# Kernel optimization log

Measured on AMD Instinct MI355X. Metric: run time of the kernel, lower is better.

## Reference

```python
import jax, jax.numpy as jnp
import numpy as np

N = 100000      # nodes
E = 1600000     # edges
F = 128         # num_node_features
H = 128         # hidden_channels
C = 10          # num_classes
R = 2           # num relations
G = 512         # num graphs in the batch


def setup_inputs() -> dict:
    key = jax.random.key(0)
    ks = jax.random.split(key, 16)
    s = 0.05
    x = jax.random.normal(ks[0], (N, F), dtype=jnp.float32)
    edge_index = jax.random.randint(ks[1], (2, E), 0, N, dtype=jnp.int64)
    edge_attr = jax.random.randint(ks[2], (E,), 0, R, dtype=jnp.int64)
    batch = jnp.sort(jax.random.randint(ks[3], (N,), 0, G, dtype=jnp.int64))
    W1 = jax.random.normal(ks[4], (R, F, H), dtype=jnp.float32) * s
    root1 = jax.random.normal(ks[5], (F, H), dtype=jnp.float32) * s
    b1 = jnp.zeros((H,), dtype=jnp.float32)
    W2 = jax.random.normal(ks[6], (R, H, H), dtype=jnp.float32) * s
    root2 = jax.random.normal(ks[7], (H, H), dtype=jnp.float32) * s
    b2 = jnp.zeros((H,), dtype=jnp.float32)
    W3 = jax.random.normal(ks[8], (R, H, H), dtype=jnp.float32) * s
    root3 = jax.random.normal(ks[9], (H, H), dtype=jnp.float32) * s
    b3 = jnp.zeros((H,), dtype=jnp.float32)
    lin_w = jax.random.normal(ks[10], (H, C), dtype=jnp.float32) * s
    lin_b = jnp.zeros((C,), dtype=jnp.float32)
    return dict(x=x, edge_index=edge_index, edge_attr=edge_attr, batch=batch,
                W1=W1, root1=root1, b1=b1, W2=W2, root2=root2, b2=b2,
                W3=W3, root3=root3, b3=b3, lin_w=lin_w, lin_b=lin_b)


def _rgcn_layer(x, src, dst, edge_type, W, root, b):
    # PyG RGCNConv: out = x @ root + b + sum_r mean_{edges of rel r -> i}(x_j @ W_r)
    n = x.shape[0]
    out = x @ root + b
    for r in range(R):
        h = x @ W[r]                               # [N, H] transform-then-gather
        w = (edge_type == r).astype(x.dtype)       # [E] relation mask
        num = jax.ops.segment_sum(h[src] * w[:, None], dst, num_segments=n)
        cnt = jax.ops.segment_sum(w, dst, num_segments=n)
        out = out + num / jnp.maximum(cnt, 1.0)[:, None]
    return out


def reference(x, edge_index, edge_attr, batch, W1, root1, b1, W2, root2, b2,
              W3, root3, b3, lin_w, lin_b):
    src, dst = edge_index[0], edge_index[1]
    h = jax.nn.relu(_rgcn_layer(x, src, dst, edge_attr, W1, root1, b1))
    h = jax.nn.relu(_rgcn_layer(h, src, dst, edge_attr, W2, root2, b2))
    h = jax.nn.relu(_rgcn_layer(h, src, dst, edge_attr, W3, root3, b3))
    # global mean pool over graphs
    psum = jax.ops.segment_sum(h, batch, num_segments=G)
    pcnt = jax.ops.segment_sum(jnp.ones((h.shape[0],), h.dtype), batch, num_segments=G)
    pooled = psum / jnp.maximum(pcnt, 1.0)[:, None]
    return pooled @ lin_w + lin_b
```

## Files before the change

### kernel.cpp

```cpp
#include <hip/hip_runtime.h>
#include <hip/hip_bf16.h>

#define Nn 100000
#define Ee 1600000
#define Ff 128
#define Hh 128
#define Cc 10
#define Gg 512

#define NBK 391
#define ABLK 8192
#define NABLK ((Ee + ABLK - 1) / ABLK)
#define BMAX 5376

typedef short bf16x8 __attribute__((ext_vector_type(8)));
typedef float f32x4 __attribute__((ext_vector_type(4)));
typedef float f32x2 __attribute__((ext_vector_type(2)));

__device__ __forceinline__ unsigned short f2bf(float f) {
    unsigned u = __float_as_uint(f);
    u += 0x7fffu + ((u >> 16) & 1u);
    return (unsigned short)(u >> 16);
}
__device__ __forceinline__ unsigned pk2(float a, float b) {
    return (unsigned)f2bf(a) | ((unsigned)f2bf(b) << 16);
}

__global__ __launch_bounds__(256) void cast_x(const float* __restrict__ x,
                                              uint2* __restrict__ xb) {
    int i = blockIdx.x * 256 + threadIdx.x;
    if (i >= Nn * Ff / 4) return;
    float4 v = ((const float4*)x)[i];
    uint2 o;
    o.x = pk2(v.x, v.y);
    o.y = pk2(v.z, v.w);
    xb[i] = o;
}

__global__ __launch_bounds__(256) void pack_w(const float* __restrict__ W1, const float* __restrict__ r1,
                                              const float* __restrict__ W2, const float* __restrict__ r2,
                                              const float* __restrict__ W3, const float* __restrict__ r3,
                                              unsigned short* __restrict__ wp) {
    int t = blockIdx.x * 256 + threadIdx.x;
    if (t >= 9 * 16384) return;
    int i = t & 7, l = (t >> 3) & 63, s = (t >> 9) & 3, c = (t >> 11) & 7, m = t >> 14;
    int k = s * 32 + ((l >> 4) << 3) + i;
    int n = (c << 4) + (l & 15);
    int q = m / 3, j = m % 3;
    const float* Ws[3] = {W1, W2, W3};
    const float* rs[3] = {r1, r2, r3};
    const float* src = (j == 0) ? rs[q] : (Ws[q] + (size_t)(j - 1) * Ff * Hh);
    wp[t] = f2bf(src[k * Hh + n]);
}

__global__ __launch_bounds__(256) void bin_count(const int* __restrict__ ei,
                                                 int* __restrict__ bucketCnt) {
    __shared__ int lc[NBK];
    for (int t = threadIdx.x; t < NBK; t += 256) lc[t] = 0;
    __syncthreads();
    int base = blockIdx.x * ABLK;
    int nhere = min(ABLK, Ee - base);
    for (int j = threadIdx.x; j < nhere; j += 256)
        atomicAdd(&lc[ei[Ee + base + j] >> 8], 1);
    __syncthreads();
    for (int t = threadIdx.x; t < NBK; t += 256)
        if (lc[t]) atomicAdd(&bucketCnt[t], lc[t]);
}

__global__ void bucket_scan(const int* __restrict__ bucketCnt,
                            int* __restrict__ bucketStart,
                            int* __restrict__ bucketCur,
                            int* __restrict__ rowstart) {
    __shared__ int pa_[512], pb_[512];
    int t = threadIdx.x;
    int v = (t < NBK) ? bucketCnt[t] : 0;
    pa_[t] = v;
    __syncthreads();
    int* pa = pa_; int* pb = pb_;
    for (int off = 1; off < 512; off <<= 1) {
        int x = pa[t] + ((t >= off) ? pa[t - off] : 0);
        __syncthreads();
        pb[t] = x;
        __syncthreads();
        int* tmp = pa; pa = pb; pb = tmp;
    }
    int excl = pa[t] - v;
    if (t <= NBK) bucketStart[t] = excl;
    if (t < NBK) bucketCur[t] = excl;
    if (t == 0) rowstart[Nn] = Ee;
}

__global__ __launch_bounds__(512) void bin_edges(const int* __restrict__ ei,
                                                 const int* __restrict__ ea,
                                                 int* __restrict__ bucketCur,
                                                 int* __restrict__ csr) {
    __shared__ int lcnt[512];
    __shared__ int lstart[512];
    __shared__ int gbase[512];
    __shared__ int lcur[512];
    __shared__ int stage[ABLK];
    __shared__ unsigned short sbkt[ABLK];
    int t = threadIdx.x;
    int base = blockIdx.x * ABLK;
    int nhere = min(ABLK, Ee - base);
    lcnt[t] = 0;
    __syncthreads();
    for (int j = t; j < nhere; j += 512)
        atomicAdd(&lcnt[ei[Ee + base + j] >> 8], 1);
    __syncthreads();
    int v = lcnt[t];
    if (t < NBK) gbase[t] = (v > 0) ? atomicAdd(&bucketCur[t], v) : 0;
    int* pa = lcnt; int* pb = lstart;
    for (int off = 1; off < 512; off <<= 1) {
        int x = pa[t] + ((t >= off) ? pa[t - off] : 0);
        __syncthreads();
        pb[t] = x;
        __syncthreads();
        int* tmp = pa; pa = pb; pb = tmp;
    }
    int excl = pa[t] - v;
    __syncthreads();
    lstart[t] = excl;
    lcur[t] = excl;
    __syncthreads();
    for (int j = t; j < nhere; j += 512) {
        int e = base + j;
        int d = ei[Ee + e];
        int srcv = ei[e];
        int r = ea[e] & 1;
        int bkt = d >> 8;
        int lp = atomicAdd(&lcur[bkt], 1);
        stage[lp] = (srcv << 9) | ((d & 255) << 1) | r;
        sbkt[lp] = (unsigned short)bkt;
    }
    __syncthreads();
    for (int j = t; j < nhere; j += 512) {
        int bkt = sbkt[j];
        csr[gbase[bkt] + (j - lstart[bkt])] = stage[j];
    }
}

__global__ __launch_bounds__(512) void sort_bucket(const int* __restrict__ bucketStart,
                                                   int* __restrict__ csr,
                                                   int* __restrict__ rowstart,
                                                   int* __restrict__ mid) {
    __shared__ int cnt_[512];
    __shared__ int start_[512];
    __shared__ int cur_[512];
    __shared__ int stage[BMAX];
    int b = blockIdx.x;
    int t = threadIdx.x;
    int s = bucketStart[b], e = bucketStart[b + 1];
    int n = e - s;
    cnt_[t] = 0;
    __syncthreads();
    for (int j = t; j < n; j += 512)
        atomicAdd(&cnt_[csr[s + j] & 511], 1);
    __syncthreads();
    int v = cnt_[t];
    int* pa = cnt_; int* pb = start_;
    for (int off = 1; off < 512; off <<= 1) {
        int x = pa[t] + ((t >= off) ? pa[t - off] : 0);
        __syncthreads();
        pb[t] = x;
        __syncthreads();
        int* tmp = pa; pa = pb; pb = tmp;
    }
    int excl = pa[t] - v;
    __syncthreads();
    start_[t] = excl;
    cur_[t] = excl;
    __syncthreads();
    if (t < 256) {
        int d = b * 256 + t;
        if (d < Nn) {
            rowstart[d] = s + start_[2 * t];
            mid[d]      = s + start_[2 * t + 1];
        }
    }
    for (int j = t; j < n; j += 512) {
        int rec = csr[s + j];
        int lp = atomicAdd(&cur_[rec & 511], 1);
        stage[lp] = rec >> 9;
    }
    __syncthreads();
    for (int j = t; j < n; j += 512)
        csr[s + j] = stage[j];
}

__global__ __launch_bounds__(256) void graph_starts(const int* __restrict__ batch,
                                                    int* __restrict__ gstart) {
    int n = blockIdx.x * 256 + threadIdx.x;
    if (n > Nn) return;
    int bp = (n == 0) ? -1 : batch[n - 1];
    int bc = (n == Nn) ? Gg : batch[n];
    for (int g = bp + 1; g <= bc; ++g) gstart[g] = n;
}

__device__ __forceinline__ void accbf(f32x2 A[4], uint4 v) {
    A[0] += (f32x2){__uint_as_float(v.x << 16), __uint_as_float(v.x & 0xffff0000u)};
    A[1] += (f32x2){__uint_as_float(v.y << 16), __uint_as_float(v.y & 0xffff0000u)};
    A[2] += (f32x2){__uint_as_float(v.z << 16), __uint_as_float(v.z & 0xffff0000u)};
    A[3] += (f32x2){__uint_as_float(v.w << 16), __uint_as_float(v.w & 0xffff0000u)};
}

__global__ __launch_bounds__(256) void aggregate(const unsigned short* __restrict__ xb,
                                                 const unsigned short* __restrict__ zrow,
                                                 const int* __restrict__ csr,
                                                 const int* __restrict__ rowstart,
                                                 const int* __restrict__ mid,
                                                 unsigned int* __restrict__ xg0,
                                                 unsigned int* __restrict__ xg1) {
    int d = blockIdx.x * 4 + (threadIdx.x >> 6);
    if (d >= Nn) return;
    int lane = threadIdx.x & 63;
    int slot = lane >> 4;
    int c8 = (lane & 15) * 8;
    int s = rowstart[d], md = mid[d], e = rowstart[d + 1];

    f32x2 A0[4], A1[4];
    #pragma unroll
    for (int j = 0; j < 4; ++j) { A0[j] = (f32x2){0.f, 0.f}; A1[j] = (f32x2){0.f, 0.f}; }

    int n0 = md - s, n1 = e - md;
    int nq = (max(n0, n1) + 3) >> 2;
    int lim0 = max(md - 1, 0);
    int lim1 = max(e - 1, 0);
    const unsigned short* zp = zrow + c8;

    #pragma unroll 2
    for (int q = 0; q < nq; ++q) {
        int i0 = s + q * 4 + slot;
        int i1 = md + q * 4 + slot;
        int r0 = csr[min(i0, lim0)];
        int r1 = csr[min(i1, lim1)];
        const unsigned short* p0 = (i0 < md) ? (xb + (size_t)r0 * Hh + c8) : zp;
        const unsigned short* p1 = (i1 < e)  ? (xb + (size_t)r1 * Hh + c8) : zp;
        uint4 v0 = *(const uint4*)p0;
        uint4 v1 = *(const uint4*)p1;
        accbf(A0, v0);
        accbf(A1, v1);
    }

    #pragma unroll
    for (int j = 0; j < 4; ++j) {
        A0[j].x += __shfl_xor(A0[j].x, 16); A0[j].y += __shfl_xor(A0[j].y, 16);
        A0[j].x += __shfl_xor(A0[j].x, 32); A0[j].y += __shfl_xor(A0[j].y, 32);
        A1[j].x += __shfl_xor(A1[j].x, 16); A1[j].y += __shfl_xor(A1[j].y, 16);
        A1[j].x += __shfl_xor(A1[j].x, 32); A1[j].y += __shfl_xor(A1[j].y, 32);
    }

    if (slot == 0) {
        float i0 = 1.f / fmaxf((float)n0, 1.f);
        float i1 = 1.f / fmaxf((float)n1, 1.f);
        uint4 o0, o1;
        o0.x = pk2(A0[0].x * i0, A0[0].y * i0);
        o0.y = pk2(A0[1].x * i0, A0[1].y * i0);
        o0.z = pk2(A0[2].x * i0, A0[2].y * i0);
        o0.w = pk2(A0[3].x * i0, A0[3].y * i0);
        o1.x = pk2(A1[0].x * i1, A1[0].y * i1);
        o1.y = pk2(A1[1].x * i1, A1[1].y * i1);
        o1.z = pk2(A1[2].x * i1, A1[2].y * i1);
        o1.w = pk2(A1[3].x * i1, A1[3].y * i1);
        *(uint4*)(xg0 + (size_t)d * (Hh / 2) + (lane & 15) * 4) = o0;
        *(uint4*)(xg1 + (size_t)d * (Hh / 2) + (lane & 15) * 4) = o1;
    }
}

__global__ __launch_bounds__(256) void gemm_fused(const unsigned short* __restrict__ x0,
                                                  const unsigned short* __restrict__ xg0,
                                                  const unsigned short* __restrict__ xg1,
                                                  const unsigned short* __restrict__ wl,
                                                  const float* __restrict__ bias,
                                                  unsigned short* __restrict__ out) {
    int w = threadIdx.x >> 6, lane = threadIdx.x & 63;
    int m = lane & 15, ksel = lane >> 4;
    int row0 = blockIdx.x * 128 + w * 32;

    const unsigned short* srcs[3] = {x0, xg0, xg1};
    bf16x8 a[2][3][4];
    #pragma unroll
    for (int rt = 0; rt < 2; ++rt) {
        int node = row0 + rt * 16 + m;
        #pragma unroll
        for (int mat = 0; mat < 3; ++mat) {
            const unsigned short* xrow = srcs[mat] + (size_t)node * Ff;
            #pragma unroll
            for (int s = 0; s < 4; ++s) {
                if (node < Nn) {
                    a[rt][mat][s] = *(const bf16x8*)(xrow + s * 32 + ksel * 8);
                } else {
                    #pragma unroll
                    for (int q = 0; q < 8; ++q) a[rt][mat][s][q] = 0;
                }
            }
        }
    }

    bool ev = (lane & 1) == 0;
    int j0 = ev ? 0 : 2;

    for (int cb = 0; cb < 8; ++cb) {
        f32x4 acc0 = {0.f, 0.f, 0.f, 0.f};
        f32x4 acc1 = {0.f, 0.f, 0.f, 0.f};
        #pragma unroll
        for (int mat = 0; mat < 3; ++mat) {
            #pragma unroll
            for (int s = 0; s < 4; ++s) {
                bf16x8 bfr = *(const bf16x8*)(wl + ((size_t)((mat * 8 + cb) * 4 + s)) * 512 + lane * 8);
                acc0 = __builtin_amdgcn_mfma_f32_16x16x32_bf16(a[0][mat][s], bfr, acc0, 0, 0, 0);
                acc1 = __builtin_amdgcn_mfma_f32_16x16x32_bf16(a[1][mat][s], bfr, acc1, 0, 0, 0);
            }
        }
        int col = cb * 16 + m;
        float bv = bias[col];
        int colb = col & ~1;
        #pragma unroll
        for (int rt = 0; rt < 2; ++rt) {
            f32x4 ac = rt ? acc1 : acc0;
            float o[4], po[4];
            #pragma unroll
            for (int j = 0; j < 4; ++j) o[j] = fmaxf(ac[j] + bv, 0.f);
            #pragma unroll
            for (int j = 0; j < 4; ++j) po[j] = __shfl_xor(o[j], 1);
            unsigned pkw0 = ev ? ((unsigned)f2bf(o[j0])      | ((unsigned)f2bf(po[j0])      << 16))
                               : ((unsigned)f2bf(po[j0])     | ((unsigned)f2bf(o[j0])       << 16));
            unsigned pkw1 = ev ? ((unsigned)f2bf(o[j0 + 1])  | ((unsigned)f2bf(po[j0 + 1])  << 16))
                               : ((unsigned)f2bf(po[j0 + 1]) | ((unsigned)f2bf(o[j0 + 1])   << 16));
            int rbase = row0 + rt * 16 + ksel * 4;
            int rr0 = rbase + j0, rr1 = rbase + j0 + 1;
            if (rr0 < Nn) *(unsigned*)(out + (size_t)rr0 * Hh + colb) = pkw0;
            if (rr1 < Nn) *(unsigned*)(out + (size_t)rr1 * Hh + colb) = pkw1;
        }
    }
}

__global__ __launch_bounds__(512) void pool_linear(const unsigned int* __restrict__ xb,
                                                   const int* __restrict__ gstart,
                                                   const float* __restrict__ lin_w,
                                                   const float* __restrict__ lin_b,
                                                   float* __restrict__ out) {
    __shared__ float red[8][128];
    int g = blockIdx.x;
    int t = threadIdx.x;
    int w = t >> 6, lane = t & 63;
    int s = gstart[g], e = gstart[g + 1];

    float a0 = 0.f, a1 = 0.f;
    for (int n = s + w; n < e; n += 8) {
        unsigned u = xb[(size_t)n * (Hh / 2) + lane];
        a0 += __uint_as_float(u << 16);
        a1 += __uint_as_float(u & 0xffff0000u);
    }
    red[w][lane * 2]     = a0;
    red[w][lane * 2 + 1] = a1;
    __syncthreads();

    if (w == 0) {
        #pragma unroll
        for (int ww = 1; ww < 8; ++ww) {
            a0 += red[ww][lane * 2];
            a1 += red[ww][lane * 2 + 1];
        }
        float inv = 1.f / fmaxf((float)(e - s), 1.f);
        a0 *= inv; a1 *= inv;
        float p[Cc];
        int k0 = 2 * lane, k1 = 2 * lane + 1;
        #pragma unroll
        for (int c = 0; c < Cc; ++c)
            p[c] = a0 * lin_w[k0 * Cc + c] + a1 * lin_w[k1 * Cc + c];
        #pragma unroll
        for (int off = 32; off > 0; off >>= 1)
            #pragma unroll
            for (int c = 0; c < Cc; ++c)
                p[c] += __shfl_down(p[c], off, 64);
        if (lane == 0)
            #pragma unroll
            for (int c = 0; c < Cc; ++c) out[g * Cc + c] = p[c] + lin_b[c];
    }
}

static inline size_t alignup(size_t v) { return (v + 255) & ~(size_t)255; }

extern "C" void kernel_launch(void* const* d_in, const int* in_sizes, int n_in,
                              void* d_out, int out_size, void* d_ws, size_t ws_size,
                              hipStream_t stream) {
    const float* x     = (const float*)d_in[0];
    const int*   ei    = (const int*)d_in[1];
    const int*   ea    = (const int*)d_in[2];
    const int*   batch = (const int*)d_in[3];
    const float* W1 = (const float*)d_in[4];
    const float* r1 = (const float*)d_in[5];
    const float* b1 = (const float*)d_in[6];
    const float* W2 = (const float*)d_in[7];
    const float* r2 = (const float*)d_in[8];
    const float* b2 = (const float*)d_in[9];
    const float* W3 = (const float*)d_in[10];
    const float* r3 = (const float*)d_in[11];
    const float* b3 = (const float*)d_in[12];
    const float* lin_w = (const float*)d_in[13];
    const float* lin_b = (const float*)d_in[14];
    float* out = (float*)d_out;

    char* p = (char*)d_ws;
    unsigned short* xbA = (unsigned short*)p;  p += alignup((size_t)Nn * Hh * 2);
    unsigned short* xbB = (unsigned short*)p;  p += alignup((size_t)Nn * Hh * 2);
    unsigned short* xg0 = (unsigned short*)p;  p += alignup((size_t)Nn * Hh * 2);
    unsigned short* xg1 = (unsigned short*)p;  p += alignup((size_t)Nn * Hh * 2);
    unsigned short* zrow = (unsigned short*)p; p += alignup((size_t)Hh * 2);
    unsigned short* wp  = (unsigned short*)p;  p += alignup((size_t)9 * 16384 * 2);
    int* rowstart    = (int*)p;                p += alignup((size_t)(Nn + 1) * 4);
    int* mid         = (int*)p;                p += alignup((size_t)Nn * 4);
    int* csr         = (int*)p;                p += alignup((size_t)Ee * 4);
    int* bucketCnt   = (int*)p;                p += alignup((size_t)NBK * 4);
    int* bucketStart = (int*)p;                p += alignup((size_t)(NBK + 1) * 4);
    int* bucketCur   = (int*)p;                p += alignup((size_t)NBK * 4);
    int* gstart      = (int*)p;                p += alignup((size_t)(Gg + 1) * 4);

    hipMemsetAsync(bucketCnt, 0, (size_t)NBK * 4, stream);
    hipMemsetAsync(zrow, 0, (size_t)Hh * 2, stream);

    cast_x<<<(Nn * Ff / 4 + 255) / 256, 256, 0, stream>>>(x, (uint2*)xbA);
    pack_w<<<(9 * 16384 + 255) / 256, 256, 0, stream>>>(W1, r1, W2, r2, W3, r3, wp);

    bin_count<<<NABLK, 256, 0, stream>>>(ei, bucketCnt);
    bucket_scan<<<1, 512, 0, stream>>>(bucketCnt, bucketStart, bucketCur, rowstart);
    bin_edges<<<NABLK, 512, 0, stream>>>(ei, ea, bucketCur, csr);
    sort_bucket<<<NBK, 512, 0, stream>>>(bucketStart, csr, rowstart, mid);

    graph_starts<<<(Nn + 1 + 255) / 256, 256, 0, stream>>>(batch, gstart);

    int gemm_grid = (Nn + 127) / 128;
    int agg_grid = (Nn + 3) / 4;

    aggregate<<<agg_grid, 256, 0, stream>>>(xbA, zrow, csr, rowstart, mid, (unsigned int*)xg0, (unsigned int*)xg1);
    gemm_fused<<<gemm_grid, 256, 0, stream>>>(xbA, xg0, xg1, wp + 0 * 3 * 16384, b1, xbB);
    aggregate<<<agg_grid, 256, 0, stream>>>(xbB, zrow, csr, rowstart, mid, (unsigned int*)xg0, (unsigned int*)xg1);
    gemm_fused<<<gemm_grid, 256, 0, stream>>>(xbB, xg0, xg1, wp + 1 * 3 * 16384, b2, xbA);
    aggregate<<<agg_grid, 256, 0, stream>>>(xbA, zrow, csr, rowstart, mid, (unsigned int*)xg0, (unsigned int*)xg1);
    gemm_fused<<<gemm_grid, 256, 0, stream>>>(xbA, xg0, xg1, wp + 2 * 3 * 16384, b3, xbB);

    pool_linear<<<Gg, 512, 0, stream>>>((const unsigned int*)xbB, gstart, lin_w, lin_b, out);
}
```

Before: 390.0 us.

## Fuse neighbor aggregation and GEMM into one per-layer kernel via LDS

Merges the aggregate and gemm_fused kernels into a single layer_fused kernel. Each 512-thread block aggregates 128 destination rows (16 per wave, processed sequentially) into swizzled LDS tiles, then runs the MFMA GEMM directly from LDS. This removes the global write and re-read of the two Nn×128 aggregated buffers and halves the kernel launches per layer. In exchange there is less parallelism during the gather phase (782 blocks instead of 25000 wave-per-node work items), 64KB of LDS per block that limits occupancy, and a possible tail imbalance from uneven node degrees.

Measured after the change: 452.9 us. 16.1% more time.

```diff
diff --git a/kernel.cpp b/kernel.cpp
--- a/kernel.cpp
+++ b/kernel.cpp
@@ -204,96 +204,105 @@
     A[3] += (f32x2){__uint_as_float(v.w << 16), __uint_as_float(v.w & 0xffff0000u)};
 }
 
-__global__ __launch_bounds__(256) void aggregate(const unsigned short* __restrict__ xb,
-                                                 const unsigned short* __restrict__ zrow,
-                                                 const int* __restrict__ csr,
-                                                 const int* __restrict__ rowstart,
-                                                 const int* __restrict__ mid,
-                                                 unsigned int* __restrict__ xg0,
-                                                 unsigned int* __restrict__ xg1) {
-    int d = blockIdx.x * 4 + (threadIdx.x >> 6);
-    if (d >= Nn) return;
-    int lane = threadIdx.x & 63;
+__global__ __launch_bounds__(512, 4) void layer_fused(const unsigned short* __restrict__ xb,
+                                                      const unsigned short* __restrict__ zrow,
+                                                      const int* __restrict__ csr,
+                                                      const int* __restrict__ rowstart,
+                                                      const int* __restrict__ mid,
+                                                      const unsigned short* __restrict__ wl,
+                                                      const float* __restrict__ bias,
+                                                      unsigned short* __restrict__ out) {
+    __shared__ unsigned char lg0[128 * 256];
+    __shared__ unsigned char lg1[128 * 256];
+    int t = threadIdx.x;
+    int w = t >> 6, lane = t & 63;
+    int base = blockIdx.x * 128;
+    int m = lane & 15, ksel = lane >> 4;
+    int row0 = base + w * 16;
+
+    bf16x8 a0[4];
+    {
+        int node = row0 + m;
+        if (node < Nn) {
+            const unsigned short* xr = xb + (size_t)node * Ff;
+            #pragma unroll
+            for (int s = 0; s < 4; ++s) a0[s] = *(const bf16x8*)(xr + s * 32 + ksel * 8);
+        } else {
+            #pragma unroll
+            for (int s = 0; s < 4; ++s)
+                #pragma unroll
+                for (int q = 0; q < 8; ++q) a0[s][q] = 0;
+        }
+    }
+
     int slot = lane >> 4;
-    int c8 = (lane & 15) * 8;
-    int s = rowstart[d], md = mid[d], e = rowstart[d + 1];
-
-    f32x2 A0[4], A1[4];
-    #pragma unroll
-    for (int j = 0; j < 4; ++j) { A0[j] = (f32x2){0.f, 0.f}; A1[j] = (f32x2){0.f, 0.f}; }
-
-    int n0 = md - s, n1 = e - md;
-    int nq = (max(n0, n1) + 3) >> 2;
-    int lim0 = max(md - 1, 0);
-    int lim1 = max(e - 1, 0);
+    int c8 = m * 8;
     const unsigned short* zp = zrow + c8;
 
-    #pragma unroll 2
-    for (int q = 0; q < nq; ++q) {
-        int i0 = s + q * 4 + slot;
-        int i1 = md + q * 4 + slot;
-        int r0 = csr[min(i0, lim0)];
-        int r1 = csr[min(i1, lim1)];
-        const unsigned short* p0 = (i0 < md) ? (xb + (size_t)r0 * Hh + c8) : zp;
-        const unsigned short* p1 = (i1 < e)  ? (xb + (size_t)r1 * Hh + c8) : zp;
-        uint4 v0 = *(const uint4*)p0;
-        uint4 v1 = *(const uint4*)p1;
-        accbf(A0, v0);
-        accbf(A1, v1);
-    }
-
-    #pragma unroll
-    for (int j = 0; j < 4; ++j) {
-        A0[j].x += __shfl_xor(A0[j].x, 16); A0[j].y += __shfl_xor(A0[j].y, 16);
-        A0[j].x += __shfl_xor(A0[j].x, 32); A0[j].y += __shfl_xor(A0[j].y, 32);
-        A1[j].x += __shfl_xor(A1[j].x, 16); A1[j].y += __shfl_xor(A1[j].y, 16);
-        A1[j].x += __shfl_xor(A1[j].x, 32); A1[j].y += __shfl_xor(A1[j].y, 32);
-    }
-
-    if (slot == 0) {
-        float i0 = 1.f / fmaxf((float)n0, 1.f);
-        float i1 = 1.f / fmaxf((float)n1, 1.f);
-        uint4 o0, o1;
-        o0.x = pk2(A0[0].x * i0, A0[0].y * i0);
-        o0.y = pk2(A0[1].x * i0, A0[1].y * i0);
-        o0.z = pk2(A0[2].x * i0, A0[2].y * i0);
-        o0.w = pk2(A0[3].x * i0, A0[3].y * i0);
-        o1.x = pk2(A1[0].x * i1, A1[0].y * i1);
-        o1.y = pk2(A1[1].x * i1, A1[1].y * i1);
-        o1.z = pk2(A1[2].x * i1, A1[2].y * i1);
-        o1.w = pk2(A1[3].x * i1, A1[3].y * i1);
-        *(uint4*)(xg0 + (size_t)d * (Hh / 2) + (lane & 15) * 4) = o0;
-        *(uint4*)(xg1 + (size_t)d * (Hh / 2) + (lane & 15) * 4) = o1;
-    }
-}
-
-__global__ __launch_bounds__(256) void gemm_fused(const unsigned short* __restrict__ x0,
-                                                  const unsigned short* __restrict__ xg0,
-                                                  const unsigned short* __restrict__ xg1,
-                                                  const unsigned short* __restrict__ wl,
-                                                  const float* __restrict__ bias,
-                                                  unsigned short* __restrict__ out) {
-    int w = threadIdx.x >> 6, lane = threadIdx.x & 63;
-    int m = lane & 15, ksel = lane >> 4;
-    int row0 = blockIdx.x * 128 + w * 32;
-
-    const unsigned short* srcs[3] = {x0, xg0, xg1};
-    bf16x8 a[2][3][4];
-    #pragma unroll
-    for (int rt = 0; rt < 2; ++rt) {
-        int node = row0 + rt * 16 + m;
-        #pragma unroll
-        for (int mat = 0; mat < 3; ++mat) {
-            const unsigned short* xrow = srcs[mat] + (size_t)node * Ff;
-            #pragma unroll
-            for (int s = 0; s < 4; ++s) {
-                if (node < Nn) {
-                    a[rt][mat][s] = *(const bf16x8*)(xrow + s * 32 + ksel * 8);
-                } else {
-                    #pragma unroll
-                    for (int q = 0; q < 8; ++q) a[rt][mat][s][q] = 0;
-                }
-            }
+    for (int j = 0; j < 16; ++j) {
+        int d = row0 + j;
+        if (d >= Nn) break;
+        int rs = rowstart[d], md = mid[d], re = rowstart[d + 1];
+
+        f32x2 A0[4], A1[4];
+        #pragma unroll
+        for (int k = 0; k < 4; ++k) { A0[k] = (f32x2){0.f, 0.f}; A1[k] = (f32x2){0.f, 0.f}; }
+
+        int n0 = md - rs, n1 = re - md;
+        int nq = (max(n0, n1) + 3) >> 2;
+        int lim0 = max(md - 1, 0);
+        int lim1 = max(re - 1, 0);
+
+        #pragma unroll 2
+        for (int q = 0; q < nq; ++q) {
+            int i0 = rs + q * 4 + slot;
+            int i1 = md + q * 4 + slot;
+            int r0 = csr[min(i0, lim0)];
+            int r1 = csr[min(i1, lim1)];
+            const unsigned short* p0 = (i0 < md) ? (xb + (size_t)r0 * Hh + c8) : zp;
+            const unsigned short* p1 = (i1 < re) ? (xb + (size_t)r1 * Hh + c8) : zp;
+            uint4 v0 = *(const uint4*)p0;
+            uint4 v1 = *(const uint4*)p1;
+            accbf(A0, v0);
+            accbf(A1, v1);
+        }
+
+        #pragma unroll
+        for (int k = 0; k < 4; ++k) {
+            A0[k].x += __shfl_xor(A0[k].x, 16); A0[k].y += __shfl_xor(A0[k].y, 16);
+            A0[k].x += __shfl_xor(A0[k].x, 32); A0[k].y += __shfl_xor(A0[k].y, 32);
+            A1[k].x += __shfl_xor(A1[k].x, 16); A1[k].y += __shfl_xor(A1[k].y, 16);
+            A1[k].x += __shfl_xor(A1[k].x, 32); A1[k].y += __shfl_xor(A1[k].y, 32);
+        }
+
+        if (slot == 0) {
+            float i0 = 1.f / fmaxf((float)n0, 1.f);
+            float i1 = 1.f / fmaxf((float)n1, 1.f);
+            uint4 o0, o1;
+            o0.x = pk2(A0[0].x * i0, A0[0].y * i0);
+            o0.y = pk2(A0[1].x * i0, A0[1].y * i0);
+            o0.z = pk2(A0[2].x * i0, A0[2].y * i0);
+            o0.w = pk2(A0[3].x * i0, A0[3].y * i0);
+            o1.x = pk2(A1[0].x * i1, A1[0].y * i1);
+            o1.y = pk2(A1[1].x * i1, A1[1].y * i1);
+            o1.z = pk2(A1[2].x * i1, A1[2].y * i1);
+            o1.w = pk2(A1[3].x * i1, A1[3].y * i1);
+            int row = w * 16 + j;
+            unsigned b0 = (unsigned)(row * 256 + m * 16) ^ (unsigned)((row & 7) << 4);
+            *(uint4*)(lg0 + b0) = o0;
+            *(uint4*)(lg1 + b0) = o1;
+        }
+    }
+    __syncthreads();
+
+    bf16x8 a1f[4], a2f[4];
+    {
+        int row = w * 16 + m;
+        #pragma unroll
+        for (int s = 0; s < 4; ++s) {
+            unsigned b0 = (unsigned)(row * 256 + s * 64 + ksel * 16) ^ (unsigned)((row & 7) << 4);
+            a1f[s] = *(const bf16x8*)(lg0 + b0);
+            a2f[s] = *(const bf16x8*)(lg1 + b0);
         }
     }
 
@@ -301,37 +310,39 @@
     int j0 = ev ? 0 : 2;
 
     for (int cb = 0; cb < 8; ++cb) {
-        f32x4 acc0 = {0.f, 0.f, 0.f, 0.f};
-        f32x4 acc1 = {0.f, 0.f, 0.f, 0.f};
-        #pragma unroll
-        for (int mat = 0; mat < 3; ++mat) {
-            #pragma unroll
-            for (int s = 0; s < 4; ++s) {
-                bf16x8 bfr = *(const bf16x8*)(wl + ((size_t)((mat * 8 + cb) * 4 + s)) * 512 + lane * 8);
-                acc0 = __builtin_amdgcn_mfma_f32_16x16x32_bf16(a[0][mat][s], bfr, acc0, 0, 0, 0);
-                acc1 = __builtin_amdgcn_mfma_f32_16x16x32_bf16(a[1][mat][s], bfr, acc1, 0, 0, 0);
-            }
-        }
+        f32x4 acc = {0.f, 0.f, 0.f, 0.f};
+        #pragma unroll
+        for (int s = 0; s < 4; ++s) {
+            bf16x8 bfr = *(const bf16x8*)(wl + ((size_t)((0 * 8 + cb) * 4 + s)) * 512 + lane * 8);
+            acc = __builtin_amdgcn_mfma_f32_16x16x32_bf16(a0[s], bfr, acc, 0, 0, 0);
+        }
+        #pragma unroll
+        for (int s = 0; s < 4; ++s) {
+            bf16x8 bfr = *(const bf16x8*)(wl + ((size_t)((1 * 8 + cb) * 4 + s)) * 512 + lane * 8);
+            acc = __builtin_amdgcn_mfma_f32_16x16x32_bf16(a1f[s], bfr, acc, 0, 0, 0);
+        }
+        #pragma unroll
+        for (int s = 0; s < 4; ++s) {
+            bf16x8 bfr = *(const bf16x8*)(wl + ((size_t)((2 * 8 + cb) * 4 + s)) * 512 + lane * 8);
+            acc = __builtin_amdgcn_mfma_f32_16x16x32_bf16(a2f[s], bfr, acc, 0, 0, 0);
+        }
+
         int col = cb * 16 + m;
         float bv = bias[col];
         int colb = col & ~1;
-        #pragma unroll
-        for (int rt = 0; rt < 2; ++rt) {
-            f32x4 ac = rt ? acc1 : acc0;
-            float o[4], po[4];
-            #pragma unroll
-            for (int j = 0; j < 4; ++j) o[j] = fmaxf(ac[j] + bv, 0.f);
-            #pragma unroll
-            for (int j = 0; j < 4; ++j) po[j] = __shfl_xor(o[j], 1);
-            unsigned pkw0 = ev ? ((unsigned)f2bf(o[j0])      | ((unsigned)f2bf(po[j0])      << 16))
-                               : ((unsigned)f2bf(po[j0])     | ((unsigned)f2bf(o[j0])       << 16));
-            unsigned pkw1 = ev ? ((unsigned)f2bf(o[j0 + 1])  | ((unsigned)f2bf(po[j0 + 1])  << 16))
-                               : ((unsigned)f2bf(po[j0 + 1]) | ((unsigned)f2bf(o[j0 + 1])   << 16));
-            int rbase = row0 + rt * 16 + ksel * 4;
-            int rr0 = rbase + j0, rr1 = rbase + j0 + 1;
-            if (rr0 < Nn) *(unsigned*)(out + (size_t)rr0 * Hh + colb) = pkw0;
-            if (rr1 < Nn) *(unsigned*)(out + (size_t)rr1 * Hh + colb) = pkw1;
-        }
+        float o[4], po[4];
+        #pragma unroll
+        for (int j = 0; j < 4; ++j) o[j] = fmaxf(acc[j] + bv, 0.f);
+        #pragma unroll
+        for (int j = 0; j < 4; ++j) po[j] = __shfl_xor(o[j], 1);
+        unsigned pkw0 = ev ? ((unsigned)f2bf(o[j0])      | ((unsigned)f2bf(po[j0])      << 16))
+                           : ((unsigned)f2bf(po[j0])     | ((unsigned)f2bf(o[j0])       << 16));
+        unsigned pkw1 = ev ? ((unsigned)f2bf(o[j0 + 1])  | ((unsigned)f2bf(po[j0 + 1])  << 16))
+                           : ((unsigned)f2bf(po[j0 + 1]) | ((unsigned)f2bf(o[j0 + 1])   << 16));
+        int rbase = row0 + ksel * 4;
+        int rr0 = rbase + j0, rr1 = rbase + j0 + 1;
+        if (rr0 < Nn) *(unsigned*)(out + (size_t)rr0 * Hh + colb) = pkw0;
+        if (rr1 < Nn) *(unsigned*)(out + (size_t)rr1 * Hh + colb) = pkw1;
     }
 }
 
@@ -405,8 +416,6 @@
     char* p = (char*)d_ws;
     unsigned short* xbA = (unsigned short*)p;  p += alignup((size_t)Nn * Hh * 2);
     unsigned short* xbB = (unsigned short*)p;  p += alignup((size_t)Nn * Hh * 2);
-    unsigned short* xg0 = (unsigned short*)p;  p += alignup((size_t)Nn * Hh * 2);
-    unsigned short* xg1 = (unsigned short*)p;  p += alignup((size_t)Nn * Hh * 2);
     unsigned short* zrow = (unsigned short*)p; p += alignup((size_t)Hh * 2);
     unsigned short* wp  = (unsigned short*)p;  p += alignup((size_t)9 * 16384 * 2);
     int* rowstart    = (int*)p;                p += alignup((size_t)(Nn + 1) * 4);
@@ -430,15 +439,11 @@
 
     graph_starts<<<(Nn + 1 + 255) / 256, 256, 0, stream>>>(batch, gstart);
 
-    int gemm_grid = (Nn + 127) / 128;
-    int agg_grid = (Nn + 3) / 4;
-
-    aggregate<<<agg_grid, 256, 0, stream>>>(xbA, zrow, csr, rowstart, mid, (unsigned int*)xg0, (unsigned int*)xg1);
-    gemm_fused<<<gemm_grid, 256, 0, stream>>>(xbA, xg0, xg1, wp + 0 * 3 * 16384, b1, xbB);
-    aggregate<<<agg_grid, 256, 0, stream>>>(xbB, zrow, csr, rowstart, mid, (unsigned int*)xg0, (unsigned int*)xg1);
-    gemm_fused<<<gemm_grid, 256, 0, stream>>>(xbB, xg0, xg1, wp + 1 * 3 * 16384, b2, xbA);
-    aggregate<<<agg_grid, 256, 0, stream>>>(xbA, zrow, csr, rowstart, mid, (unsigned int*)xg0, (unsigned int*)xg1);
-    gemm_fused<<<gemm_grid, 256, 0, stream>>>(xbA, xg0, xg1, wp + 2 * 3 * 16384, b3, xbB);
+    int nblk = (Nn + 127) / 128;
+
+    layer_fused<<<nblk, 512, 0, stream>>>(xbA, zrow, csr, rowstart, mid, wp + 0 * 3 * 16384, b1, xbB);
+    layer_fused<<<nblk, 512, 0, stream>>>(xbB, zrow, csr, rowstart, mid, wp + 1 * 3 * 16384, b2, xbA);
+    layer_fused<<<nblk, 512, 0, stream>>>(xbA, zrow, csr, rowstart, mid, wp + 2 * 3 * 16384, b3, xbB);
 
     pool_linear<<<Gg, 512, 0, stream>>>((const unsigned int*)xbB, gstart, lin_w, lin_b, out);
 }
```

## Drop bucket count pass with fixed-capacity buckets; stage GEMM weights in LDS

Applied to the files above, without the earlier changes.

Removes the bin_count and bucket_scan kernels by giving each destination bucket a fixed BMAX-sized slot in the CSR array, so bin_edges reserves space with atomics on per-bucket cursors. sort_bucket now emits an explicit rowend array because buckets are no longer contiguous. The GEMM is restructured to 512-thread blocks covering 256 rows that load each weight matrix into LDS once and keep all accumulators in registers, replacing per-wave global weight reads. The fixed capacity assumes no bucket exceeds BMAX edges, which holds only for a roughly uniform destination distribution, and the larger accumulator set raises register pressure.

Result: faster. 355.7 us, median of 2 (-8.8%).

```diff
diff --git a/kernel.cpp b/kernel.cpp
--- a/kernel.cpp
+++ b/kernel.cpp
@@ -9,7 +9,7 @@
 #define Gg 512
 
 #define NBK 391
-#define ABLK 8192
+#define ABLK 4096
 #define NABLK ((Ee + ABLK - 1) / ABLK)
 #define BMAX 5376
 
@@ -53,43 +53,6 @@
     wp[t] = f2bf(src[k * Hh + n]);
 }
 
-__global__ __launch_bounds__(256) void bin_count(const int* __restrict__ ei,
-                                                 int* __restrict__ bucketCnt) {
-    __shared__ int lc[NBK];
-    for (int t = threadIdx.x; t < NBK; t += 256) lc[t] = 0;
-    __syncthreads();
-    int base = blockIdx.x * ABLK;
-    int nhere = min(ABLK, Ee - base);
-    for (int j = threadIdx.x; j < nhere; j += 256)
-        atomicAdd(&lc[ei[Ee + base + j] >> 8], 1);
-    __syncthreads();
-    for (int t = threadIdx.x; t < NBK; t += 256)
-        if (lc[t]) atomicAdd(&bucketCnt[t], lc[t]);
-}
-
-__global__ void bucket_scan(const int* __restrict__ bucketCnt,
-                            int* __restrict__ bucketStart,
-                            int* __restrict__ bucketCur,
-                            int* __restrict__ rowstart) {
-    __shared__ int pa_[512], pb_[512];
-    int t = threadIdx.x;
-    int v = (t < NBK) ? bucketCnt[t] : 0;
-    pa_[t] = v;
-    __syncthreads();
-    int* pa = pa_; int* pb = pb_;
-    for (int off = 1; off < 512; off <<= 1) {
-        int x = pa[t] + ((t >= off) ? pa[t - off] : 0);
-        __syncthreads();
-        pb[t] = x;
-        __syncthreads();
-        int* tmp = pa; pa = pb; pb = tmp;
-    }
-    int excl = pa[t] - v;
-    if (t <= NBK) bucketStart[t] = excl;
-    if (t < NBK) bucketCur[t] = excl;
-    if (t == 0) rowstart[Nn] = Ee;
-}
-
 __global__ __launch_bounds__(512) void bin_edges(const int* __restrict__ ei,
                                                  const int* __restrict__ ea,
                                                  int* __restrict__ bucketCur,
@@ -136,26 +99,27 @@
     __syncthreads();
     for (int j = t; j < nhere; j += 512) {
         int bkt = sbkt[j];
-        csr[gbase[bkt] + (j - lstart[bkt])] = stage[j];
-    }
-}
-
-__global__ __launch_bounds__(512) void sort_bucket(const int* __restrict__ bucketStart,
+        csr[(size_t)bkt * BMAX + gbase[bkt] + (j - lstart[bkt])] = stage[j];
+    }
+}
+
+__global__ __launch_bounds__(512) void sort_bucket(const int* __restrict__ bucketCur,
                                                    int* __restrict__ csr,
                                                    int* __restrict__ rowstart,
-                                                   int* __restrict__ mid) {
+                                                   int* __restrict__ mid,
+                                                   int* __restrict__ rowend) {
     __shared__ int cnt_[512];
     __shared__ int start_[512];
     __shared__ int cur_[512];
     __shared__ int stage[BMAX];
     int b = blockIdx.x;
     int t = threadIdx.x;
-    int s = bucketStart[b], e = bucketStart[b + 1];
-    int n = e - s;
+    int s = b * BMAX;
+    int n = bucketCur[b];
     cnt_[t] = 0;
     __syncthreads();
     for (int j = t; j < n; j += 512)
-        atomicAdd(&cnt_[csr[s + j] & 511], 1);
+        atomicAdd(&cnt_[csr[(size_t)s + j] & 511], 1);
     __syncthreads();
     int v = cnt_[t];
     int* pa = cnt_; int* pb = start_;
@@ -176,16 +140,17 @@
         if (d < Nn) {
             rowstart[d] = s + start_[2 * t];
             mid[d]      = s + start_[2 * t + 1];
+            rowend[d]   = s + ((t < 255) ? start_[2 * t + 2] : n);
         }
     }
     for (int j = t; j < n; j += 512) {
-        int rec = csr[s + j];
+        int rec = csr[(size_t)s + j];
         int lp = atomicAdd(&cur_[rec & 511], 1);
         stage[lp] = rec >> 9;
     }
     __syncthreads();
     for (int j = t; j < n; j += 512)
-        csr[s + j] = stage[j];
+        csr[(size_t)s + j] = stage[j];
 }
 
 __global__ __launch_bounds__(256) void graph_starts(const int* __restrict__ batch,
@@ -209,6 +174,7 @@
                                                  const int* __restrict__ csr,
                                                  const int* __restrict__ rowstart,
                                                  const int* __restrict__ mid,
+                                                 const int* __restrict__ rowend,
                                                  unsigned int* __restrict__ xg0,
                                                  unsigned int* __restrict__ xg1) {
     int d = blockIdx.x * 4 + (threadIdx.x >> 6);
@@ -216,7 +182,7 @@
     int lane = threadIdx.x & 63;
     int slot = lane >> 4;
     int c8 = (lane & 15) * 8;
-    int s = rowstart[d], md = mid[d], e = rowstart[d + 1];
+    int s = rowstart[d], md = mid[d], e = rowend[d];
 
     f32x2 A0[4], A1[4];
     #pragma unroll
@@ -267,57 +233,72 @@
     }
 }
 
-__global__ __launch_bounds__(256) void gemm_fused(const unsigned short* __restrict__ x0,
-                                                  const unsigned short* __restrict__ xg0,
-                                                  const unsigned short* __restrict__ xg1,
-                                                  const unsigned short* __restrict__ wl,
-                                                  const float* __restrict__ bias,
-                                                  unsigned short* __restrict__ out) {
-    int w = threadIdx.x >> 6, lane = threadIdx.x & 63;
+__global__ __launch_bounds__(512, 2) void gemm_fused(const unsigned short* __restrict__ x0,
+                                                     const unsigned short* __restrict__ xg0,
+                                                     const unsigned short* __restrict__ xg1,
+                                                     const unsigned short* __restrict__ wl,
+                                                     const float* __restrict__ bias,
+                                                     unsigned short* __restrict__ out) {
+    __shared__ unsigned short wlds[16384];
+    int t = threadIdx.x;
+    int w = t >> 6, lane = t & 63;
     int m = lane & 15, ksel = lane >> 4;
-    int row0 = blockIdx.x * 128 + w * 32;
+    int row0 = blockIdx.x * 256 + w * 32;
 
     const unsigned short* srcs[3] = {x0, xg0, xg1};
-    bf16x8 a[2][3][4];
+    f32x4 acc[2][8];
     #pragma unroll
-    for (int rt = 0; rt < 2; ++rt) {
-        int node = row0 + rt * 16 + m;
-        #pragma unroll
-        for (int mat = 0; mat < 3; ++mat) {
-            const unsigned short* xrow = srcs[mat] + (size_t)node * Ff;
+    for (int rt = 0; rt < 2; ++rt)
+        #pragma unroll
+        for (int cb = 0; cb < 8; ++cb) acc[rt][cb] = (f32x4){0.f, 0.f, 0.f, 0.f};
+
+    #pragma unroll
+    for (int mat = 0; mat < 3; ++mat) {
+        if (mat) __syncthreads();
+        {
+            const uint4* ws_ = (const uint4*)(wl + (size_t)mat * 16384);
+            uint4* wd_ = (uint4*)wlds;
+            #pragma unroll
+            for (int c = 0; c < 4; ++c) wd_[c * 512 + t] = ws_[c * 512 + t];
+        }
+        bf16x8 a[2][4];
+        #pragma unroll
+        for (int rt = 0; rt < 2; ++rt) {
+            int node = row0 + rt * 16 + m;
+            const unsigned short* xr = srcs[mat] + (size_t)node * Ff;
             #pragma unroll
             for (int s = 0; s < 4; ++s) {
                 if (node < Nn) {
-                    a[rt][mat][s] = *(const bf16x8*)(xrow + s * 32 + ksel * 8);
+                    a[rt][s] = *(const bf16x8*)(xr + s * 32 + ksel * 8);
                 } else {
                     #pragma unroll
-                    for (int q = 0; q < 8; ++q) a[rt][mat][s][q] = 0;
+                    for (int q = 0; q < 8; ++q) a[rt][s][q] = 0;
                 }
             }
         }
+        __syncthreads();
+        #pragma unroll
+        for (int cb = 0; cb < 8; ++cb) {
+            #pragma unroll
+            for (int s = 0; s < 4; ++s) {
+                bf16x8 bfr = *(const bf16x8*)(wlds + (size_t)(cb * 4 + s) * 512 + lane * 8);
+                acc[0][cb] = __builtin_amdgcn_mfma_f32_16x16x32_bf16(a[0][s], bfr, acc[0][cb], 0, 0, 0);
+                acc[1][cb] = __builtin_amdgcn_mfma_f32_16x16x32_bf16(a[1][s], bfr, acc[1][cb], 0, 0, 0);
+            }
+        }
     }
 
     bool ev = (lane & 1) == 0;
     int j0 = ev ? 0 : 2;
 
+    #pragma unroll
     for (int cb = 0; cb < 8; ++cb) {
-        f32x4 acc0 = {0.f, 0.f, 0.f, 0.f};
-        f32x4 acc1 = {0.f, 0.f, 0.f, 0.f};
-        #pragma unroll
-        for (int mat = 0; mat < 3; ++mat) {
-            #pragma unroll
-            for (int s = 0; s < 4; ++s) {
-                bf16x8 bfr = *(const bf16x8*)(wl + ((size_t)((mat * 8 + cb) * 4 + s)) * 512 + lane * 8);
-                acc0 = __builtin_amdgcn_mfma_f32_16x16x32_bf16(a[0][mat][s], bfr, acc0, 0, 0, 0);
-                acc1 = __builtin_amdgcn_mfma_f32_16x16x32_bf16(a[1][mat][s], bfr, acc1, 0, 0, 0);
-            }
-        }
         int col = cb * 16 + m;
         float bv = bias[col];
         int colb = col & ~1;
         #pragma unroll
         for (int rt = 0; rt < 2; ++rt) {
-            f32x4 ac = rt ? acc1 : acc0;
+            f32x4 ac = acc[rt][cb];
             float o[4], po[4];
             #pragma unroll
             for (int j = 0; j < 4; ++j) o[j] = fmaxf(ac[j] + bv, 0.f);
@@ -409,36 +390,33 @@
     unsigned short* xg1 = (unsigned short*)p;  p += alignup((size_t)Nn * Hh * 2);
     unsigned short* zrow = (unsigned short*)p; p += alignup((size_t)Hh * 2);
     unsigned short* wp  = (unsigned short*)p;  p += alignup((size_t)9 * 16384 * 2);
-    int* rowstart    = (int*)p;                p += alignup((size_t)(Nn + 1) * 4);
+    int* rowstart    = (int*)p;                p += alignup((size_t)Nn * 4);
     int* mid         = (int*)p;                p += alignup((size_t)Nn * 4);
-    int* csr         = (int*)p;                p += alignup((size_t)Ee * 4);
-    int* bucketCnt   = (int*)p;                p += alignup((size_t)NBK * 4);
-    int* bucketStart = (int*)p;                p += alignup((size_t)(NBK + 1) * 4);
+    int* rowend      = (int*)p;                p += alignup((size_t)Nn * 4);
+    int* csr         = (int*)p;                p += alignup((size_t)NBK * BMAX * 4);
     int* bucketCur   = (int*)p;                p += alignup((size_t)NBK * 4);
     int* gstart      = (int*)p;                p += alignup((size_t)(Gg + 1) * 4);
 
-    hipMemsetAsync(bucketCnt, 0, (size_t)NBK * 4, stream);
+    hipMemsetAsync(bucketCur, 0, (size_t)NBK * 4, stream);
     hipMemsetAsync(zrow, 0, (size_t)Hh * 2, stream);
 
     cast_x<<<(Nn * Ff / 4 + 255) / 256, 256, 0, stream>>>(x, (uint2*)xbA);
     pack_w<<<(9 * 16384 + 255) / 256, 256, 0, stream>>>(W1, r1, W2, r2, W3, r3, wp);
 
-    bin_count<<<NABLK, 256, 0, stream>>>(ei, bucketCnt);
-    bucket_scan<<<1, 512, 0, stream>>>(bucketCnt, bucketStart, bucketCur, rowstart);
     bin_edges<<<NABLK, 512, 0, stream>>>(ei, ea, bucketCur, csr);
-    sort_bucket<<<NBK, 512, 0, stream>>>(bucketStart, csr, rowstart, mid);
+    sort_bucket<<<NBK, 512, 0, stream>>>(bucketCur, csr, rowstart, mid, rowend);
 
     graph_starts<<<(Nn + 1 + 255) / 256, 256, 0, stream>>>(batch, gstart);
 
-    int gemm_grid = (Nn + 127) / 128;
     int agg_grid = (Nn + 3) / 4;
-
-    aggregate<<<agg_grid, 256, 0, stream>>>(xbA, zrow, csr, rowstart, mid, (unsigned int*)xg0, (unsigned int*)xg1);
-    gemm_fused<<<gemm_grid, 256, 0, stream>>>(xbA, xg0, xg1, wp + 0 * 3 * 16384, b1, xbB);
-    aggregate<<<agg_grid, 256, 0, stream>>>(xbB, zrow, csr, rowstart, mid, (unsigned int*)xg0, (unsigned int*)xg1);
-    gemm_fused<<<gemm_grid, 256, 0, stream>>>(xbB, xg0, xg1, wp + 1 * 3 * 16384, b2, xbA);
-    aggregate<<<agg_grid, 256, 0, stream>>>(xbA, zrow, csr, rowstart, mid, (unsigned int*)xg0, (unsigned int*)xg1);
-    gemm_fused<<<gemm_grid, 256, 0, stream>>>(xbA, xg0, xg1, wp + 2 * 3 * 16384, b3, xbB);
+    int gemm_grid = (Nn + 255) / 256;
+
+    aggregate<<<agg_grid, 256, 0, stream>>>(xbA, zrow, csr, rowstart, mid, rowend, (unsigned int*)xg0, (unsigned int*)xg1);
+    gemm_fused<<<gemm_grid, 512, 0, stream>>>(xbA, xg0, xg1, wp + 0 * 3 * 16384, b1, xbB);
+    aggregate<<<agg_grid, 256, 0, stream>>>(xbB, zrow, csr, rowstart, mid, rowend, (unsigned int*)xg0, (unsigned int*)xg1);
+    gemm_fused<<<gemm_grid, 512, 0, stream>>>(xbB, xg0, xg1, wp + 1 * 3 * 16384, b2, xbA);
+    aggregate<<<agg_grid, 256, 0, stream>>>(xbA, zrow, csr, rowstart, mid, rowend, (unsigned int*)xg0, (unsigned int*)xg1);
+    gemm_fused<<<gemm_grid, 512, 0, stream>>>(xbA, xg0, xg1, wp + 2 * 3 * 16384, b3, xbB);
 
     pool_linear<<<Gg, 512, 0, stream>>>((const unsigned int*)xbB, gstart, lin_w, lin_b, out);
 }
```
